# Kernel tuning notes

Hardware: AMD Instinct MI355X
Metric: run time of the kernel (lower is better)

## Reference

```python
import jax, jax.numpy as jnp
import numpy as np

DIM = 768
HEADS = 12
HD = DIM // HEADS
E = 8
R = 64
ALPHA = 128.0
LORA_SCALE = ALPHA / R  # 2.0
ENABLE_BITS = np.array([1.0, 0.0, 1.0], dtype=np.float32)  # LoRA on q and v slices of qkv


def setup_inputs() -> dict:
    key = jax.random.key(0)
    ks = jax.random.split(key, 8)
    x = jax.random.normal(ks[0], (2, 4096, DIM), jnp.float32)
    # base (frozen) weights, shared across experts; no biases (qkv_bias=False)
    Wqkv = jax.random.normal(ks[1], (3 * DIM, DIM), jnp.float32) * 0.02
    Wproj = jax.random.normal(ks[2], (DIM, DIM), jnp.float32) * 0.02
    # per-expert LoRA adapters. qkv: shared down-proj A, per-output-slice up-proj B,
    # masked by enable bits (q,k,v).
    Aqkv = jax.random.normal(ks[3], (E, R, DIM), jnp.float32) * 0.02
    Bqkv = jax.random.normal(ks[4], (E, 3, DIM, R), jnp.float32) * 0.02
    Bqkv = Bqkv * jnp.asarray(ENABLE_BITS)[None, :, None, None]
    Aproj = jax.random.normal(ks[5], (E, R, DIM), jnp.float32) * 0.02
    Bproj = jax.random.normal(ks[6], (E, DIM, R), jnp.float32) * 0.02
    expert_indices = np.arange(4, dtype=np.int64) % E  # static per-chunk routing
    chunk_sizes = np.array([1024, 1024, 1024, 1024], dtype=np.int64)
    return {"x": x, "Wqkv": Wqkv, "Aqkv": Aqkv, "Bqkv": Bqkv, "Wproj": Wproj,
            "Aproj": Aproj, "Bproj": Bproj, "expert_indices": expert_indices,
            "chunk_sizes": chunk_sizes}


def reference(x, Wqkv, Aqkv, Bqkv, Wproj, Aproj, Bproj, expert_indices, chunk_sizes):
    # chunk sizes / expert indices are static host-side routing metadata
    sizes = [int(c) for c in np.asarray(chunk_sizes)]
    eidx = [int(e) for e in np.asarray(expert_indices)]
    offs = np.concatenate([[0], np.cumsum(sizes)])
    B = x.shape[0]
    scale = HD ** -0.5
    last_k = None
    last_v = None
    outs = []
    for i, n in enumerate(sizes):
        xc = x[:, offs[i]:offs[i + 1]]            # [B, n, DIM]
        e = eidx[i]
        # LoRA-adapted qkv for this chunk's expert
        base = xc @ Wqkv.T                        # [B, n, 3*DIM]
        h = xc @ Aqkv[e].T                        # [B, n, R]
        delta = jnp.einsum('bnr,tdr->bntd', h, Bqkv[e]).reshape(B, n, 3 * DIM)
        qkv = (base + LORA_SCALE * delta).reshape(B, n, 3, HEADS, HD)
        qkv = qkv.transpose(2, 0, 3, 1, 4)        # [3, B, H, n, HD]
        q, k, v = qkv[0], qkv[1], qkv[2]
        if last_k is not None:                    # growing KV over chunks (chunk-causal)
            k = jnp.concatenate([last_k, k], axis=-2)
            v = jnp.concatenate([last_v, v], axis=-2)
        last_k, last_v = k, v
        attn = jax.nn.softmax(jnp.einsum('bhqd,bhkd->bhqk', q * scale, k), axis=-1)
        o = jnp.einsum('bhqk,bhkd->bhqd', attn, v)
        o = o.transpose(0, 2, 1, 3).reshape(B, n, DIM)
        # LoRA-adapted output projection for the same expert
        o = o @ Wproj.T + LORA_SCALE * ((o @ Aproj[e].T) @ Bproj[e].T)
        outs.append(o)
    return jnp.concatenate(outs, axis=1)          # [B, total, DIM]
```

## Files before the change

### kernel.cpp

```cpp
#include <hip/hip_runtime.h>
#include <math.h>

#define BATCH   2
#define SEQ     4096
#define DIMD    768
#define NHEADS  12
#define HDIM    64
#define RR      64
#define CHUNK   1024
#define NTOK    (BATCH * SEQ)
#define BHN     (BATCH * NHEADS)
#define KC2     2304
#define QSCALE  0.18033688011112042f

typedef __attribute__((ext_vector_type(8))) short short8;
typedef __attribute__((ext_vector_type(4))) float f32x4;

#define AS1 __attribute__((address_space(1)))
#define AS3 __attribute__((address_space(3)))

__device__ __forceinline__ void glds16(const void* g, void* l) {
    __builtin_amdgcn_global_load_lds((const AS1 unsigned int*)g,
                                     (AS3 unsigned int*)l, 16, 0, 0);
}

__device__ __forceinline__ unsigned short f2bf(float x) {
    union { float f; unsigned u; } c; c.f = x;
    unsigned u = c.u + 0x7fffu + ((c.u >> 16) & 1u);
    return (unsigned short)(u >> 16);
}
__device__ __forceinline__ float bf2f(unsigned short h) {
    union { unsigned u; float f; } c; c.u = ((unsigned)h) << 16;
    return c.f;
}
__device__ __forceinline__ unsigned pack2bf(float a, float b) {
    union { float f; unsigned u; } x, y; x.f = a; y.f = b;
    unsigned ua = x.u + 0x7fffu + ((x.u >> 16) & 1u);
    unsigned ub = y.u + 0x7fffu + ((y.u >> 16) & 1u);
    return (ua >> 16) | (ub & 0xffff0000u);
}

__global__ __launch_bounds__(256)
void combine_split(const float* __restrict__ W, const float* __restrict__ A,
                   const float* __restrict__ Bm, int NB,
                   unsigned short* __restrict__ out)
{
    const int tid = threadIdx.x;
    const int ty = tid >> 4, tx = tid & 15;
    const int f0 = blockIdx.x * 64, d0 = blockIdx.y * 64, e = blockIdx.z;

    __shared__ float Bb[64][68];
    __shared__ float Aa[64][68];

    const float* Ae = A + (long)e * RR * DIMD;
    const float* Be = Bm + (long)e * NB * RR;

    const int lrow = tid >> 2, lc = (tid & 3) * 16;
    #pragma unroll
    for (int u = 0; u < 16; u += 4) {
        *(float4*)&Bb[lrow][lc + u] = *(const float4*)&Be[(long)(f0 + lrow) * RR + lc + u];
        *(float4*)&Aa[lrow][lc + u] = *(const float4*)&Ae[(long)lrow * DIMD + d0 + lc + u];
    }
    __syncthreads();

    float acc[4][4] = {};
    #pragma unroll 4
    for (int r = 0; r < RR; r++) {
        const float4 bv = *(float4*)&Aa[r][tx * 4];
        #pragma unroll
        for (int i = 0; i < 4; i++) {
            const float av = Bb[ty + 16 * i][r];
            acc[i][0] = fmaf(av, bv.x, acc[i][0]);
            acc[i][1] = fmaf(av, bv.y, acc[i][1]);
            acc[i][2] = fmaf(av, bv.z, acc[i][2]);
            acc[i][3] = fmaf(av, bv.w, acc[i][3]);
        }
    }

    #pragma unroll
    for (int i = 0; i < 4; i++) {
        const int f = f0 + ty + 16 * i;
        const int d = d0 + tx * 4;
        unsigned short* o = out + ((long)e * NB + f) * KC2 + d;
        const float4 wv = *(const float4*)&W[(long)f * DIMD + d];
        const float v0 = wv.x + 2.0f * acc[i][0];
        const float v1 = wv.y + 2.0f * acc[i][1];
        const float v2 = wv.z + 2.0f * acc[i][2];
        const float v3 = wv.w + 2.0f * acc[i][3];
        const unsigned short h0 = f2bf(v0), h1 = f2bf(v1);
        const unsigned short h2 = f2bf(v2), h3 = f2bf(v3);
        uint2 hp, lp;
        hp.x = (unsigned)h0 | ((unsigned)h1 << 16);
        hp.y = (unsigned)h2 | ((unsigned)h3 << 16);
        lp.x = pack2bf(v0 - bf2f(h0), v1 - bf2f(h1));
        lp.y = pack2bf(v2 - bf2f(h2), v3 - bf2f(h3));
        *(uint2*)&o[0]    = hp;
        *(uint2*)&o[768]  = lp;
        *(uint2*)&o[1536] = hp;
    }
}

__global__ __launch_bounds__(192)
void build_xa2(const float* __restrict__ X, unsigned short* __restrict__ out)
{
    const int tok = blockIdx.x;
    const int j = threadIdx.x * 4;
    const float* xr = X + (long)tok * DIMD;
    unsigned short* o = out + (long)tok * KC2;
    float4 v = *(const float4*)&xr[j];
    unsigned short h0 = f2bf(v.x), h1 = f2bf(v.y), h2 = f2bf(v.z), h3 = f2bf(v.w);
    uint2 hp, lp;
    hp.x = (unsigned)h0 | ((unsigned)h1 << 16);
    hp.y = (unsigned)h2 | ((unsigned)h3 << 16);
    lp.x = pack2bf(v.x - bf2f(h0), v.y - bf2f(h1));
    lp.y = pack2bf(v.z - bf2f(h2), v.w - bf2f(h3));
    *(uint2*)&o[j] = hp;
    *(uint2*)&o[768 + j] = hp;
    *(uint2*)&o[1536 + j] = lp;
}

template<int MODE, int NBT>
__global__ __launch_bounds__(256)
void mfma_gemm(const unsigned short* __restrict__ A,
               const unsigned short* __restrict__ B, int NB, int n_base,
               unsigned short* __restrict__ qpl, unsigned short* __restrict__ kpl,
               unsigned short* __restrict__ vpl, float* __restrict__ outf)
{
    __shared__ __align__(16) unsigned short lA[128 * 64];
    __shared__ __align__(16) unsigned short lB[128 * 64];

    const int tid = threadIdx.x;
    const int lane = tid & 63;
    const int wave = tid >> 6;
    const int n = lane & 15;
    const int quad = lane >> 4;
    const int wm = wave & 1, wn = wave >> 1;

    const int id = blockIdx.x;
    const int xcd = id & 7;
    const int loc = id >> 3;
    const int p = xcd * (NBT / 2) + (loc >> 4);
    const int ml = loc & 15;
    const int e = p / NBT;
    const int nb = p - e * NBT;
    const int mb = ((ml >> 3) << 5) + e * 8 + (ml & 7);
    const int m0 = mb * 128;
    const int n0 = n_base + nb * 128;
    const unsigned short* Ap = A + (long)m0 * KC2;
    const unsigned short* Bp = B + ((long)e * NB + n0) * KC2;

    long soff[4];
    int sldsoff = wave * 1024;
    #pragma unroll
    for (int iss = 0; iss < 4; iss++) {
        const int g = iss * 256 + tid;
        const int row = g >> 3;
        const int gc = (g & 7) ^ (row & 7);
        soff[iss] = (long)row * KC2 + gc * 8;
    }

    f32x4 acc[4][4];
    #pragma unroll
    for (int i = 0; i < 4; i++)
        #pragma unroll
        for (int j = 0; j < 4; j++)
            acc[i][j] = (f32x4){0.f, 0.f, 0.f, 0.f};

    for (int k0 = 0; k0 < KC2; k0 += 64) {
        __syncthreads();
        #pragma unroll
        for (int iss = 0; iss < 4; iss++) {
            glds16(Ap + soff[iss] + k0, (char*)lA + iss * 4096 + sldsoff);
            glds16(Bp + soff[iss] + k0, (char*)lB + iss * 4096 + sldsoff);
        }
        __builtin_amdgcn_s_waitcnt(0);
        __syncthreads();

        #pragma unroll
        for (int kk = 0; kk < 2; kk++) {
            const int kg = kk * 4;
            short8 af[4], bfr[4];
            #pragma unroll
            for (int mt = 0; mt < 4; mt++) {
                const int r = wm * 64 + mt * 16 + n;
                const int p2 = (kg + quad) ^ (r & 7);
                af[mt] = *(const short8*)&lA[r * 64 + p2 * 8];
            }
            #pragma unroll
            for (int nt = 0; nt < 4; nt++) {
                const int r = wn * 64 + nt * 16 + n;
                const int p2 = (kg + quad) ^ (r & 7);
                bfr[nt] = *(const short8*)&lB[r * 64 + p2 * 8];
            }
            #pragma unroll
            for (int mt = 0; mt < 4; mt++)
                #pragma unroll
                for (int nt = 0; nt < 4; nt++) {
                    if (MODE == 1)
                        acc[mt][nt] = __builtin_amdgcn_mfma_f32_16x16x32_bf16(
                            af[mt], bfr[nt], acc[mt][nt], 0, 0, 0);
                    else
                        acc[mt][nt] = __builtin_amdgcn_mfma_f32_16x16x32_bf16(
                            bfr[nt], af[mt], acc[mt][nt], 0, 0, 0);
                }
        }
    }

    #pragma unroll
    for (int mt = 0; mt < 4; mt++) {
        #pragma unroll
        for (int nt = 0; nt < 4; nt++) {
            f32x4 a = acc[mt][nt];
            if (MODE == 0) {
                const int fb = n0 + wn * 64 + nt * 16 + quad * 4;
                const int t = fb >= 768 ? 1 : 0;
                const int rem = fb - t * 768;
                const int head = rem >> 6;
                const int d0 = rem & 63;
                const int token = m0 + wm * 64 + mt * 16 + n;
                const int b = token >> 12, s = token & (SEQ - 1);
                const int bh = b * NHEADS + head;
                const float sc = t ? 1.0f : QSCALE;
                unsigned short* dst = (t ? kpl : qpl) + ((long)(bh * SEQ + s)) * HDIM + d0;
                uint2 pk;
                pk.x = pack2bf(a[0] * sc, a[1] * sc);
                pk.y = pack2bf(a[2] * sc, a[3] * sc);
                *(uint2*)dst = pk;
            } else if (MODE == 1) {
                const int f = n0 + wn * 64 + nt * 16 + n;
                const int head = (f - 1536) >> 6;
                const int d = f & 63;
                const int tok0 = m0 + wm * 64 + mt * 16 + quad * 4;
                const int b = tok0 >> 12, s0 = tok0 & (SEQ - 1);
                const int bh = b * NHEADS + head;
                unsigned short* dst = vpl + ((long)(bh * HDIM + d)) * SEQ + s0;
                uint2 pk;
                pk.x = pack2bf(a[0], a[1]);
                pk.y = pack2bf(a[2], a[3]);
                *(uint2*)dst = pk;
            } else {
                const int fb = n0 + wn * 64 + nt * 16 + quad * 4;
                const int token = m0 + wm * 64 + mt * 16 + n;
                *(f32x4*)&outf[(long)token * DIMD + fb] = a;
            }
        }
    }
}

__global__ __launch_bounds__(512)
void attn_split(const unsigned short* __restrict__ qp,
                const unsigned short* __restrict__ kpl,
                const unsigned short* __restrict__ vtp,
                unsigned short* __restrict__ XA,
                float* __restrict__ pO, float* __restrict__ pl)
{
    __shared__ __align__(16) unsigned short lK[64 * 64];
    __shared__ __align__(16) unsigned short lV[64 * 64];
    __shared__ __align__(16) unsigned short lP[8][32 * 64];

    const int tid = threadIdx.x;
    const int lane = tid & 63;
    const int wave = tid >> 6;
    const int n = lane & 15;
    const int quad = lane >> 4;
    const int c7 = n & 7;

    const int id = blockIdx.x;
    const int xcd = id & 7;
    const int loc = id >> 3;
    const int sub = loc % 3;
    const int r2 = loc / 3;
    const int z = r2 % 6;
    const int qb = r2 / 6;
    const int bh = xcd * 3 + sub;

    int ci, ks0, klen, pidx;
    switch (z) {
        case 0:  ci = 3; ks0 = 0;    klen = 2048; pidx = 0;  break;
        case 1:  ci = 3; ks0 = 2048; klen = 2048; pidx = 1;  break;
        case 2:  ci = 2; ks0 = 0;    klen = 2048; pidx = 2;  break;
        case 3:  ci = 1; ks0 = 0;    klen = 2048; pidx = -1; break;
        case 4:  ci = 2; ks0 = 2048; klen = 1024; pidx = 3;  break;
        default: ci = 0; ks0 = 0;    klen = 1024; pidx = -1; break;
    }
    const int b = bh / NHEADS;
    const int h = bh - b * NHEADS;

    const long planeQK = (long)bh * SEQ * HDIM;
    const long planeVt = (long)bh * HDIM * SEQ;
    const int qch = qb * 256 + wave * 32;
    const int q0 = ci * CHUNK + qch;

    long skoff, svoff;
    {
        const int row = tid >> 3;
        const int gc = (tid & 7) ^ (row & 7);
        skoff = (long)row * HDIM + gc * 8;
        svoff = (long)row * SEQ + gc * 8;
    }

    short8 qf[2][2];
    #pragma unroll
    for (int qt = 0; qt < 2; qt++)
        #pragma unroll
        for (int s = 0; s < 2; s++)
            qf[qt][s] = *(const short8*)&qp[planeQK + (long)(q0 + qt * 16 + n) * HDIM + s * 32 + quad * 8];

    const short8 ones8 = {0x3f80, 0x3f80, 0x3f80, 0x3f80, 0x3f80, 0x3f80, 0x3f80, 0x3f80};

    f32x4 acc[4][2];
    f32x4 accl[2];
    #pragma unroll
    for (int m2 = 0; m2 < 4; m2++) {
        acc[m2][0] = (f32x4){0.f, 0.f, 0.f, 0.f};
        acc[m2][1] = (f32x4){0.f, 0.f, 0.f, 0.f};
    }
    accl[0] = (f32x4){0.f, 0.f, 0.f, 0.f};
    accl[1] = (f32x4){0.f, 0.f, 0.f, 0.f};

    unsigned short* Pw = &lP[wave][0];

    for (int k0 = ks0; k0 < ks0 + klen; k0 += 64) {
        __syncthreads();
        glds16(kpl + planeQK + (long)k0 * HDIM + skoff, (char*)lK + wave * 1024);
        glds16(vtp + planeVt + k0 + svoff, (char*)lV + wave * 1024);
        __builtin_amdgcn_s_waitcnt(0);
        __syncthreads();

        f32x4 st[4][2];
        #pragma unroll
        for (int kt = 0; kt < 4; kt++) {
            st[kt][0] = (f32x4){0.f, 0.f, 0.f, 0.f};
            st[kt][1] = (f32x4){0.f, 0.f, 0.f, 0.f};
        }
        #pragma unroll
        for (int s = 0; s < 2; s++) {
            #pragma unroll
            for (int kt = 0; kt < 4; kt++) {
                const int gr = (s * 4 + quad) ^ c7;
                short8 kf = *(const short8*)&lK[(kt * 16 + n) * 64 + gr * 8];
                st[kt][0] = __builtin_amdgcn_mfma_f32_16x16x32_bf16(kf, qf[0][s], st[kt][0], 0, 0, 0);
                st[kt][1] = __builtin_amdgcn_mfma_f32_16x16x32_bf16(kf, qf[1][s], st[kt][1], 0, 0, 0);
            }
        }

        #pragma unroll
        for (int qt = 0; qt < 2; qt++) {
            unsigned short* prow = Pw + (qt * 16 + n) * 64;
            #pragma unroll
            for (int kt = 0; kt < 4; kt++) {
                const unsigned u0 = __float_as_uint(__builtin_exp2f(st[kt][qt][0])) + 0x8000u;
                const unsigned u1 = __float_as_uint(__builtin_exp2f(st[kt][qt][1])) + 0x8000u;
                const unsigned u2 = __float_as_uint(__builtin_exp2f(st[kt][qt][2])) + 0x8000u;
                const unsigned u3 = __float_as_uint(__builtin_exp2f(st[kt][qt][3])) + 0x8000u;
                uint2 pkv;
                pkv.x = __builtin_amdgcn_perm(u1, u0, 0x07060302);
                pkv.y = __builtin_amdgcn_perm(u3, u2, 0x07060302);
                const int gsw = (2 * kt + (quad >> 1)) ^ c7;
                *(uint2*)&prow[gsw * 8 + (quad & 1) * 4] = pkv;
            }
        }

        #pragma unroll
        for (int hh = 0; hh < 2; hh++) {
            short8 pf[2];
            #pragma unroll
            for (int qt = 0; qt < 2; qt++) {
                const int gsw = (hh * 4 + quad) ^ c7;
                pf[qt] = *(const short8*)&Pw[(qt * 16 + n) * 64 + gsw * 8];
            }
            #pragma unroll
            for (int m2 = 0; m2 < 4; m2++) {
                const int gr = (hh * 4 + quad) ^ c7;
                short8 vf = *(const short8*)&lV[(m2 * 16 + n) * 64 + gr * 8];
                acc[m2][0] = __builtin_amdgcn_mfma_f32_16x16x32_bf16(vf, pf[0], acc[m2][0], 0, 0, 0);
                acc[m2][1] = __builtin_amdgcn_mfma_f32_16x16x32_bf16(vf, pf[1], acc[m2][1], 0, 0, 0);
            }
            accl[0] = __builtin_amdgcn_mfma_f32_16x16x32_bf16(ones8, pf[0], accl[0], 0, 0, 0);
            accl[1] = __builtin_amdgcn_mfma_f32_16x16x32_bf16(ones8, pf[1], accl[1], 0, 0, 0);
        }
    }

    if (pidx < 0) {
        #pragma unroll
        for (int qt = 0; qt < 2; qt++) {
            const float inv = 1.0f / accl[qt][0];
            const int token = b * SEQ + q0 + qt * 16 + n;
            unsigned short* xrow = XA + (long)token * KC2;
            #pragma unroll
            for (int m2 = 0; m2 < 4; m2++) {
                const int d = h * HDIM + m2 * 16 + quad * 4;
                const float o0 = acc[m2][qt][0] * inv;
                const float o1 = acc[m2][qt][1] * inv;
                const float o2 = acc[m2][qt][2] * inv;
                const float o3 = acc[m2][qt][3] * inv;
                const unsigned short h0 = f2bf(o0), h1 = f2bf(o1);
                const unsigned short h2 = f2bf(o2), h3 = f2bf(o3);
                uint2 hp, lp;
                hp.x = (unsigned)h0 | ((unsigned)h1 << 16);
                hp.y = (unsigned)h2 | ((unsigned)h3 << 16);
                lp.x = pack2bf(o0 - bf2f(h0), o1 - bf2f(h1));
                lp.y = pack2bf(o2 - bf2f(h2), o3 - bf2f(h3));
                *(uint2*)&xrow[d] = hp;
                *(uint2*)&xrow[768 + d] = hp;
                *(uint2*)&xrow[1536 + d] = lp;
            }
        }
    } else {
        const long pq = (long)(pidx * BHN + bh) * 1024 + qch;
        #pragma unroll
        for (int qt = 0; qt < 2; qt++) {
            const long qoff = (pq + qt * 16 + n) * 64;
            #pragma unroll
            for (int m2 = 0; m2 < 4; m2++)
                *(f32x4*)&pO[qoff + m2 * 16 + quad * 4] = acc[m2][qt];
            if (quad == 0)
                pl[pq + qt * 16 + n] = accl[qt][0];
        }
    }
}

__global__ __launch_bounds__(256)
void attn_combine(const float* __restrict__ pO, const float* __restrict__ pl,
                  unsigned short* __restrict__ XA)
{
    const int t = threadIdx.x;
    const int g = blockIdx.x;
    const int ci = 2 + (g >> 3);
    const int qb = g & 7;
    const int bh = blockIdx.y;
    const int b = bh / NHEADS, h = bh - b * NHEADS;
    const int pA = (ci == 2) ? 2 : 0;
    const int pB = (ci == 2) ? 3 : 1;

    const int qrow = t >> 1;
    const int dh = (t & 1) * 32;
    const int qc = qb * 128 + qrow;
    const long iA = (long)(pA * BHN + bh) * 1024 + qc;
    const long iB = (long)(pB * BHN + bh) * 1024 + qc;
    const float inv = 1.0f / (pl[iA] + pl[iB]);
    const int token = b * SEQ + ci * CHUNK + qc;
    unsigned short* xrow = XA + (long)token * KC2 + h * HDIM + dh;

    #pragma unroll
    for (int u = 0; u < 8; u++) {
        const float4 a = *(const float4*)&pO[iA * 64 + dh + u * 4];
        const float4 c = *(const float4*)&pO[iB * 64 + dh + u * 4];
        const float o0 = (a.x + c.x) * inv;
        const float o1 = (a.y + c.y) * inv;
        const float o2 = (a.z + c.z) * inv;
        const float o3 = (a.w + c.w) * inv;
        const unsigned short h0 = f2bf(o0), h1 = f2bf(o1);
        const unsigned short h2 = f2bf(o2), h3 = f2bf(o3);
        uint2 hp, lp;
        hp.x = (unsigned)h0 | ((unsigned)h1 << 16);
        hp.y = (unsigned)h2 | ((unsigned)h3 << 16);
        lp.x = pack2bf(o0 - bf2f(h0), o1 - bf2f(h1));
        lp.y = pack2bf(o2 - bf2f(h2), o3 - bf2f(h3));
        *(uint2*)&xrow[u * 4] = hp;
        *(uint2*)&xrow[768 + u * 4] = hp;
        *(uint2*)&xrow[1536 + u * 4] = lp;
    }
}

extern "C" void kernel_launch(void* const* d_in, const int* in_sizes, int n_in,
                              void* d_out, int out_size, void* d_ws, size_t ws_size,
                              hipStream_t stream) {
    (void)in_sizes; (void)n_in; (void)out_size; (void)ws_size;
    const float* x     = (const float*)d_in[0];
    const float* Wqkv  = (const float*)d_in[1];
    const float* Aqkv  = (const float*)d_in[2];
    const float* Bqkv  = (const float*)d_in[3];
    const float* Wproj = (const float*)d_in[4];
    const float* Aproj = (const float*)d_in[5];
    const float* Bproj = (const float*)d_in[6];

    char* wsb = (char*)d_ws;
    unsigned short* XA   = (unsigned short*)(wsb);
    unsigned short* WBq  = (unsigned short*)(wsb + (38l << 20));
    float*          pO   = (float*)(wsb + (38l << 20));
    float*          pl   = (float*)(wsb + (63l << 20));
    unsigned short* WBp  = (unsigned short*)(wsb + (80l << 20));
    unsigned short* qpl  = (unsigned short*)(wsb + (94l << 20));
    unsigned short* kpl  = (unsigned short*)(wsb + (107l << 20));
    unsigned short* vpl  = (unsigned short*)(wsb + (120l << 20));

    dim3 blk(256);

    combine_split<<<dim3(36, 12, 4), blk, 0, stream>>>(Wqkv, Aqkv, Bqkv, 3 * DIMD, WBq);
    combine_split<<<dim3(12, 12, 4), blk, 0, stream>>>(Wproj, Aproj, Bproj, DIMD, WBp);
    build_xa2<<<dim3(NTOK), dim3(192), 0, stream>>>(x, XA);
    mfma_gemm<0, 12><<<dim3(768), blk, 0, stream>>>(XA, WBq, 3 * DIMD, 0,    qpl, kpl, vpl, nullptr);
    mfma_gemm<1, 6><<<dim3(384),  blk, 0, stream>>>(XA, WBq, 3 * DIMD, 1536, qpl, kpl, vpl, nullptr);
    attn_split<<<dim3(576), dim3(512), 0, stream>>>(qpl, kpl, vpl, XA, pO, pl);
    attn_combine<<<dim3(16, BHN), blk, 0, stream>>>(pO, pl, XA);
    mfma_gemm<2, 6><<<dim3(384), blk, 0, stream>>>(XA, WBp, DIMD, 0, nullptr, nullptr, nullptr, (float*)d_out);
}
```

Before: 418.8 us.

## Double-buffer attention K/V, merge QKV GEMM launches, use hardware bf16 packing

The attention loop now double-buffers the K and V tiles in LDS, prefetching the next tile while the current one is computed, so it no longer waits on a load at every step. The two QKV GEMM launches are merged into one 1152-block kernel, with the shared main loop factored into a device function. The hand-written bf16 rounding helpers are replaced by the HIP __float22bfloat162_rn intrinsic, including for the softmax P packing, which was previously a cheaper round-half-up perm trick. Doubling the K/V LDS raises shared-memory use per block and may lower occupancy, and the new P packing may cost more instructions.

New measurement: 426.9 us. No clear change (+1.9%).

```diff
diff --git a/kernel.cpp b/kernel.cpp
--- a/kernel.cpp
+++ b/kernel.cpp
@@ -1,4 +1,5 @@
 #include <hip/hip_runtime.h>
+#include <hip/hip_bf16.h>
 #include <math.h>
 
 #define BATCH   2
@@ -24,21 +25,14 @@
                                      (AS3 unsigned int*)l, 16, 0, 0);
 }
 
-__device__ __forceinline__ unsigned short f2bf(float x) {
-    union { float f; unsigned u; } c; c.f = x;
-    unsigned u = c.u + 0x7fffu + ((c.u >> 16) & 1u);
-    return (unsigned short)(u >> 16);
-}
-__device__ __forceinline__ float bf2f(unsigned short h) {
-    union { unsigned u; float f; } c; c.u = ((unsigned)h) << 16;
-    return c.f;
-}
-__device__ __forceinline__ unsigned pack2bf(float a, float b) {
-    union { float f; unsigned u; } x, y; x.f = a; y.f = b;
-    unsigned ua = x.u + 0x7fffu + ((x.u >> 16) & 1u);
-    unsigned ub = y.u + 0x7fffu + ((y.u >> 16) & 1u);
-    return (ua >> 16) | (ub & 0xffff0000u);
-}
+__device__ __forceinline__ unsigned pk2u(float a, float b) {
+    float2 t; t.x = a; t.y = b;
+    __hip_bfloat162 r = __float22bfloat162_rn(t);
+    union { __hip_bfloat162 b2; unsigned u; } c; c.b2 = r;
+    return c.u;
+}
+__device__ __forceinline__ float lo16f(unsigned p) { return __uint_as_float(p << 16); }
+__device__ __forceinline__ float hi16f(unsigned p) { return __uint_as_float(p & 0xffff0000u); }
 
 __global__ __launch_bounds__(256)
 void combine_split(const float* __restrict__ W, const float* __restrict__ A,
@@ -87,13 +81,11 @@
         const float v1 = wv.y + 2.0f * acc[i][1];
         const float v2 = wv.z + 2.0f * acc[i][2];
         const float v3 = wv.w + 2.0f * acc[i][3];
-        const unsigned short h0 = f2bf(v0), h1 = f2bf(v1);
-        const unsigned short h2 = f2bf(v2), h3 = f2bf(v3);
         uint2 hp, lp;
-        hp.x = (unsigned)h0 | ((unsigned)h1 << 16);
-        hp.y = (unsigned)h2 | ((unsigned)h3 << 16);
-        lp.x = pack2bf(v0 - bf2f(h0), v1 - bf2f(h1));
-        lp.y = pack2bf(v2 - bf2f(h2), v3 - bf2f(h3));
+        hp.x = pk2u(v0, v1);
+        hp.y = pk2u(v2, v3);
+        lp.x = pk2u(v0 - lo16f(hp.x), v1 - hi16f(hp.x));
+        lp.y = pk2u(v2 - lo16f(hp.y), v3 - hi16f(hp.y));
         *(uint2*)&o[0]    = hp;
         *(uint2*)&o[768]  = lp;
         *(uint2*)&o[1536] = hp;
@@ -108,27 +100,22 @@
     const float* xr = X + (long)tok * DIMD;
     unsigned short* o = out + (long)tok * KC2;
     float4 v = *(const float4*)&xr[j];
-    unsigned short h0 = f2bf(v.x), h1 = f2bf(v.y), h2 = f2bf(v.z), h3 = f2bf(v.w);
     uint2 hp, lp;
-    hp.x = (unsigned)h0 | ((unsigned)h1 << 16);
-    hp.y = (unsigned)h2 | ((unsigned)h3 << 16);
-    lp.x = pack2bf(v.x - bf2f(h0), v.y - bf2f(h1));
-    lp.y = pack2bf(v.z - bf2f(h2), v.w - bf2f(h3));
+    hp.x = pk2u(v.x, v.y);
+    hp.y = pk2u(v.z, v.w);
+    lp.x = pk2u(v.x - lo16f(hp.x), v.y - hi16f(hp.x));
+    lp.y = pk2u(v.z - lo16f(hp.y), v.w - hi16f(hp.y));
     *(uint2*)&o[j] = hp;
     *(uint2*)&o[768 + j] = hp;
     *(uint2*)&o[1536 + j] = lp;
 }
 
-template<int MODE, int NBT>
-__global__ __launch_bounds__(256)
-void mfma_gemm(const unsigned short* __restrict__ A,
-               const unsigned short* __restrict__ B, int NB, int n_base,
-               unsigned short* __restrict__ qpl, unsigned short* __restrict__ kpl,
-               unsigned short* __restrict__ vpl, float* __restrict__ outf)
-{
-    __shared__ __align__(16) unsigned short lA[128 * 64];
-    __shared__ __align__(16) unsigned short lB[128 * 64];
-
+template<bool SWAP>
+__device__ __forceinline__ void gemm_core(const unsigned short* __restrict__ Ap,
+                                          const unsigned short* __restrict__ Bp,
+                                          unsigned short* lA, unsigned short* lB,
+                                          f32x4 acc[4][4])
+{
     const int tid = threadIdx.x;
     const int lane = tid & 63;
     const int wave = tid >> 6;
@@ -136,21 +123,8 @@
     const int quad = lane >> 4;
     const int wm = wave & 1, wn = wave >> 1;
 
-    const int id = blockIdx.x;
-    const int xcd = id & 7;
-    const int loc = id >> 3;
-    const int p = xcd * (NBT / 2) + (loc >> 4);
-    const int ml = loc & 15;
-    const int e = p / NBT;
-    const int nb = p - e * NBT;
-    const int mb = ((ml >> 3) << 5) + e * 8 + (ml & 7);
-    const int m0 = mb * 128;
-    const int n0 = n_base + nb * 128;
-    const unsigned short* Ap = A + (long)m0 * KC2;
-    const unsigned short* Bp = B + ((long)e * NB + n0) * KC2;
-
     long soff[4];
-    int sldsoff = wave * 1024;
+    const int sldsoff = wave * 1024;
     #pragma unroll
     for (int iss = 0; iss < 4; iss++) {
         const int g = iss * 256 + tid;
@@ -159,13 +133,6 @@
         soff[iss] = (long)row * KC2 + gc * 8;
     }
 
-    f32x4 acc[4][4];
-    #pragma unroll
-    for (int i = 0; i < 4; i++)
-        #pragma unroll
-        for (int j = 0; j < 4; j++)
-            acc[i][j] = (f32x4){0.f, 0.f, 0.f, 0.f};
-
     for (int k0 = 0; k0 < KC2; k0 += 64) {
         __syncthreads();
         #pragma unroll
@@ -196,22 +163,52 @@
             for (int mt = 0; mt < 4; mt++)
                 #pragma unroll
                 for (int nt = 0; nt < 4; nt++) {
-                    if (MODE == 1)
+                    if (SWAP)
+                        acc[mt][nt] = __builtin_amdgcn_mfma_f32_16x16x32_bf16(
+                            bfr[nt], af[mt], acc[mt][nt], 0, 0, 0);
+                    else
                         acc[mt][nt] = __builtin_amdgcn_mfma_f32_16x16x32_bf16(
                             af[mt], bfr[nt], acc[mt][nt], 0, 0, 0);
-                    else
-                        acc[mt][nt] = __builtin_amdgcn_mfma_f32_16x16x32_bf16(
-                            bfr[nt], af[mt], acc[mt][nt], 0, 0, 0);
                 }
         }
     }
-
-    #pragma unroll
-    for (int mt = 0; mt < 4; mt++) {
-        #pragma unroll
-        for (int nt = 0; nt < 4; nt++) {
-            f32x4 a = acc[mt][nt];
-            if (MODE == 0) {
+}
+
+__global__ __launch_bounds__(256)
+void qkv_gemm(const unsigned short* __restrict__ A, const unsigned short* __restrict__ B,
+              unsigned short* __restrict__ qpl, unsigned short* __restrict__ kpl,
+              unsigned short* __restrict__ vpl)
+{
+    __shared__ __align__(16) unsigned short lA[128 * 64];
+    __shared__ __align__(16) unsigned short lB[128 * 64];
+
+    const int tid = threadIdx.x;
+    const int lane = tid & 63;
+    const int wave = tid >> 6;
+    const int n = lane & 15;
+    const int quad = lane >> 4;
+    const int wm = wave & 1, wn = wave >> 1;
+    const int id = blockIdx.x;
+
+    f32x4 acc[4][4];
+    #pragma unroll
+    for (int i = 0; i < 4; i++)
+        #pragma unroll
+        for (int j = 0; j < 4; j++)
+            acc[i][j] = (f32x4){0.f, 0.f, 0.f, 0.f};
+
+    if (id < 768) {
+        const int xcd = id & 7, loc = id >> 3;
+        const int p = xcd * 6 + (loc >> 4), ml = loc & 15;
+        const int e = p / 12, nb = p - e * 12;
+        const int mb = ((ml >> 3) << 5) + e * 8 + (ml & 7);
+        const int m0 = mb * 128, n0 = nb * 128;
+        gemm_core<true>(A + (long)m0 * KC2, B + ((long)e * 2304 + n0) * KC2, lA, lB, acc);
+        #pragma unroll
+        for (int mt = 0; mt < 4; mt++) {
+            #pragma unroll
+            for (int nt = 0; nt < 4; nt++) {
+                f32x4 a = acc[mt][nt];
                 const int fb = n0 + wn * 64 + nt * 16 + quad * 4;
                 const int t = fb >= 768 ? 1 : 0;
                 const int rem = fb - t * 768;
@@ -223,10 +220,24 @@
                 const float sc = t ? 1.0f : QSCALE;
                 unsigned short* dst = (t ? kpl : qpl) + ((long)(bh * SEQ + s)) * HDIM + d0;
                 uint2 pk;
-                pk.x = pack2bf(a[0] * sc, a[1] * sc);
-                pk.y = pack2bf(a[2] * sc, a[3] * sc);
+                pk.x = pk2u(a[0] * sc, a[1] * sc);
+                pk.y = pk2u(a[2] * sc, a[3] * sc);
                 *(uint2*)dst = pk;
-            } else if (MODE == 1) {
+            }
+        }
+    } else {
+        const int id2 = id - 768;
+        const int xcd = id2 & 7, loc = id2 >> 3;
+        const int p = xcd * 3 + (loc >> 4), ml = loc & 15;
+        const int e = p / 6, nb = p - e * 6;
+        const int mb = ((ml >> 3) << 5) + e * 8 + (ml & 7);
+        const int m0 = mb * 128, n0 = 1536 + nb * 128;
+        gemm_core<false>(A + (long)m0 * KC2, B + ((long)e * 2304 + n0) * KC2, lA, lB, acc);
+        #pragma unroll
+        for (int mt = 0; mt < 4; mt++) {
+            #pragma unroll
+            for (int nt = 0; nt < 4; nt++) {
+                f32x4 a = acc[mt][nt];
                 const int f = n0 + wn * 64 + nt * 16 + n;
                 const int head = (f - 1536) >> 6;
                 const int d = f & 63;
@@ -235,16 +246,52 @@
                 const int bh = b * NHEADS + head;
                 unsigned short* dst = vpl + ((long)(bh * HDIM + d)) * SEQ + s0;
                 uint2 pk;
-                pk.x = pack2bf(a[0], a[1]);
-                pk.y = pack2bf(a[2], a[3]);
+                pk.x = pk2u(a[0], a[1]);
+                pk.y = pk2u(a[2], a[3]);
                 *(uint2*)dst = pk;
-            } else {
-                const int fb = n0 + wn * 64 + nt * 16 + quad * 4;
-                const int token = m0 + wm * 64 + mt * 16 + n;
-                *(f32x4*)&outf[(long)token * DIMD + fb] = a;
-            }
-        }
-    }
+            }
+        }
+    }
+}
+
+__global__ __launch_bounds__(256)
+void proj_gemm(const unsigned short* __restrict__ A, const unsigned short* __restrict__ B,
+               float* __restrict__ outf)
+{
+    __shared__ __align__(16) unsigned short lA[128 * 64];
+    __shared__ __align__(16) unsigned short lB[128 * 64];
+
+    const int tid = threadIdx.x;
+    const int lane = tid & 63;
+    const int wave = tid >> 6;
+    const int n = lane & 15;
+    const int quad = lane >> 4;
+    const int wm = wave & 1, wn = wave >> 1;
+
+    const int id = blockIdx.x;
+    const int xcd = id & 7, loc = id >> 3;
+    const int p = xcd * 3 + (loc >> 4), ml = loc & 15;
+    const int e = p / 6, nb = p - e * 6;
+    const int mb = ((ml >> 3) << 5) + e * 8 + (ml & 7);
+    const int m0 = mb * 128, n0 = nb * 128;
+
+    f32x4 acc[4][4];
+    #pragma unroll
+    for (int i = 0; i < 4; i++)
+        #pragma unroll
+        for (int j = 0; j < 4; j++)
+            acc[i][j] = (f32x4){0.f, 0.f, 0.f, 0.f};
+
+    gemm_core<true>(A + (long)m0 * KC2, B + ((long)e * 768 + n0) * KC2, lA, lB, acc);
+
+    #pragma unroll
+    for (int mt = 0; mt < 4; mt++)
+        #pragma unroll
+        for (int nt = 0; nt < 4; nt++) {
+            const int fb = n0 + wn * 64 + nt * 16 + quad * 4;
+            const int token = m0 + wm * 64 + mt * 16 + n;
+            *(f32x4*)&outf[(long)token * DIMD + fb] = acc[mt][nt];
+        }
 }
 
 __global__ __launch_bounds__(512)
@@ -254,8 +301,8 @@
                 unsigned short* __restrict__ XA,
                 float* __restrict__ pO, float* __restrict__ pl)
 {
-    __shared__ __align__(16) unsigned short lK[64 * 64];
-    __shared__ __align__(16) unsigned short lV[64 * 64];
+    __shared__ __align__(16) unsigned short lK[2 * 64 * 64];
+    __shared__ __align__(16) unsigned short lV[2 * 64 * 64];
     __shared__ __align__(16) unsigned short lP[8][32 * 64];
 
     const int tid = threadIdx.x;
@@ -290,6 +337,7 @@
     const long planeVt = (long)bh * HDIM * SEQ;
     const int qch = qb * 256 + wave * 32;
     const int q0 = ci * CHUNK + qch;
+    const int kend = ks0 + klen;
 
     long skoff, svoff;
     {
@@ -320,12 +368,21 @@
 
     unsigned short* Pw = &lP[wave][0];
 
-    for (int k0 = ks0; k0 < ks0 + klen; k0 += 64) {
-        __syncthreads();
-        glds16(kpl + planeQK + (long)k0 * HDIM + skoff, (char*)lK + wave * 1024);
-        glds16(vtp + planeVt + k0 + svoff, (char*)lV + wave * 1024);
-        __builtin_amdgcn_s_waitcnt(0);
-        __syncthreads();
+    glds16(kpl + planeQK + (long)ks0 * HDIM + skoff, (char*)lK + wave * 1024);
+    glds16(vtp + planeVt + ks0 + svoff, (char*)lV + wave * 1024);
+    __builtin_amdgcn_s_waitcnt(0);
+    __syncthreads();
+
+    int buf = 0;
+    for (int k0 = ks0; k0 < kend; k0 += 64) {
+        if (k0 + 64 < kend) {
+            glds16(kpl + planeQK + (long)(k0 + 64) * HDIM + skoff,
+                   (char*)lK + (buf ^ 1) * 8192 + wave * 1024);
+            glds16(vtp + planeVt + (k0 + 64) + svoff,
+                   (char*)lV + (buf ^ 1) * 8192 + wave * 1024);
+        }
+        const unsigned short* Kc = lK + buf * 4096;
+        const unsigned short* Vc = lV + buf * 4096;
 
         f32x4 st[4][2];
         #pragma unroll
@@ -338,7 +395,7 @@
             #pragma unroll
             for (int kt = 0; kt < 4; kt++) {
                 const int gr = (s * 4 + quad) ^ c7;
-                short8 kf = *(const short8*)&lK[(kt * 16 + n) * 64 + gr * 8];
+                short8 kf = *(const short8*)&Kc[(kt * 16 + n) * 64 + gr * 8];
                 st[kt][0] = __builtin_amdgcn_mfma_f32_16x16x32_bf16(kf, qf[0][s], st[kt][0], 0, 0, 0);
                 st[kt][1] = __builtin_amdgcn_mfma_f32_16x16x32_bf16(kf, qf[1][s], st[kt][1], 0, 0, 0);
             }
@@ -349,13 +406,9 @@
             unsigned short* prow = Pw + (qt * 16 + n) * 64;
             #pragma unroll
             for (int kt = 0; kt < 4; kt++) {
-                const unsigned u0 = __float_as_uint(__builtin_exp2f(st[kt][qt][0])) + 0x8000u;
-                const unsigned u1 = __float_as_uint(__builtin_exp2f(st[kt][qt][1])) + 0x8000u;
-                const unsigned u2 = __float_as_uint(__builtin_exp2f(st[kt][qt][2])) + 0x8000u;
-                const unsigned u3 = __float_as_uint(__builtin_exp2f(st[kt][qt][3])) + 0x8000u;
                 uint2 pkv;
-                pkv.x = __builtin_amdgcn_perm(u1, u0, 0x07060302);
-                pkv.y = __builtin_amdgcn_perm(u3, u2, 0x07060302);
+                pkv.x = pk2u(__builtin_exp2f(st[kt][qt][0]), __builtin_exp2f(st[kt][qt][1]));
+                pkv.y = pk2u(__builtin_exp2f(st[kt][qt][2]), __builtin_exp2f(st[kt][qt][3]));
                 const int gsw = (2 * kt + (quad >> 1)) ^ c7;
                 *(uint2*)&prow[gsw * 8 + (quad & 1) * 4] = pkv;
             }
@@ -372,13 +425,17 @@
             #pragma unroll
             for (int m2 = 0; m2 < 4; m2++) {
                 const int gr = (hh * 4 + quad) ^ c7;
-                short8 vf = *(const short8*)&lV[(m2 * 16 + n) * 64 + gr * 8];
+                short8 vf = *(const short8*)&Vc[(m2 * 16 + n) * 64 + gr * 8];
                 acc[m2][0] = __builtin_amdgcn_mfma_f32_16x16x32_bf16(vf, pf[0], acc[m2][0], 0, 0, 0);
                 acc[m2][1] = __builtin_amdgcn_mfma_f32_16x16x32_bf16(vf, pf[1], acc[m2][1], 0, 0, 0);
             }
             accl[0] = __builtin_amdgcn_mfma_f32_16x16x32_bf16(ones8, pf[0], accl[0], 0, 0, 0);
             accl[1] = __builtin_amdgcn_mfma_f32_16x16x32_bf16(ones8, pf[1], accl[1], 0, 0, 0);
         }
+
+        __builtin_amdgcn_s_waitcnt(0);
+        __syncthreads();
+        buf ^= 1;
     }
 
     if (pidx < 0) {
@@ -394,13 +451,11 @@
                 const float o1 = acc[m2][qt][1] * inv;
                 const float o2 = acc[m2][qt][2] * inv;
                 const float o3 = acc[m2][qt][3] * inv;
-                const unsigned short h0 = f2bf(o0), h1 = f2bf(o1);
-                const unsigned short h2 = f2bf(o2), h3 = f2bf(o3);
                 uint2 hp, lp;
-                hp.x = (unsigned)h0 | ((unsigned)h1 << 16);
-                hp.y = (unsigned)h2 | ((unsigned)h3 << 16);
-                lp.x = pack2bf(o0 - bf2f(h0), o1 - bf2f(h1));
-                lp.y = pack2bf(o2 - bf2f(h2), o3 - bf2f(h3));
+                hp.x = pk2u(o0, o1);
+                hp.y = pk2u(o2, o3);
+                lp.x = pk2u(o0 - lo16f(hp.x), o1 - hi16f(hp.x));
+                lp.y = pk2u(o2 - lo16f(hp.y), o3 - hi16f(hp.y));
                 *(uint2*)&xrow[d] = hp;
                 *(uint2*)&xrow[768 + d] = hp;
                 *(uint2*)&xrow[1536 + d] = lp;
@@ -450,13 +505,11 @@
         const float o1 = (a.y + c.y) * inv;
         const float o2 = (a.z + c.z) * inv;
         const float o3 = (a.w + c.w) * inv;
-        const unsigned short h0 = f2bf(o0), h1 = f2bf(o1);
-        const unsigned short h2 = f2bf(o2), h3 = f2bf(o3);
         uint2 hp, lp;
-        hp.x = (unsigned)h0 | ((unsigned)h1 << 16);
-        hp.y = (unsigned)h2 | ((unsigned)h3 << 16);
-        lp.x = pack2bf(o0 - bf2f(h0), o1 - bf2f(h1));
-        lp.y = pack2bf(o2 - bf2f(h2), o3 - bf2f(h3));
+        hp.x = pk2u(o0, o1);
+        hp.y = pk2u(o2, o3);
+        lp.x = pk2u(o0 - lo16f(hp.x), o1 - hi16f(hp.x));
+        lp.y = pk2u(o2 - lo16f(hp.y), o3 - hi16f(hp.y));
         *(uint2*)&xrow[u * 4] = hp;
         *(uint2*)&xrow[768 + u * 4] = hp;
         *(uint2*)&xrow[1536 + u * 4] = lp;
@@ -490,9 +543,8 @@
     combine_split<<<dim3(36, 12, 4), blk, 0, stream>>>(Wqkv, Aqkv, Bqkv, 3 * DIMD, WBq);
     combine_split<<<dim3(12, 12, 4), blk, 0, stream>>>(Wproj, Aproj, Bproj, DIMD, WBp);
     build_xa2<<<dim3(NTOK), dim3(192), 0, stream>>>(x, XA);
-    mfma_gemm<0, 12><<<dim3(768), blk, 0, stream>>>(XA, WBq, 3 * DIMD, 0,    qpl, kpl, vpl, nullptr);
-    mfma_gemm<1, 6><<<dim3(384),  blk, 0, stream>>>(XA, WBq, 3 * DIMD, 1536, qpl, kpl, vpl, nullptr);
+    qkv_gemm<<<dim3(1152), blk, 0, stream>>>(XA, WBq, qpl, kpl, vpl);
     attn_split<<<dim3(576), dim3(512), 0, stream>>>(qpl, kpl, vpl, XA, pO, pl);
     attn_combine<<<dim3(16, BHN), blk, 0, stream>>>(pO, pl, XA);
-    mfma_gemm<2, 6><<<dim3(384), blk, 0, stream>>>(XA, WBp, DIMD, 0, nullptr, nullptr, nullptr, (float*)d_out);
-}
+    proj_gemm<<<dim3(384), blk, 0, stream>>>(XA, WBp, (float*)d_out);
+}
```
